# Optimization experiments

Hardware: AMD Instinct MI355X
Metric: run time of the kernel (lower is better)

The kernel has to match this reference:

```python
import jax, jax.numpy as jnp
import numpy as np

FEATURE_SIZE = 10 * 64 * 64  # 40960
HIDDEN1 = 512
HIDDEN2 = 256
BATCH = 4096


def setup_inputs() -> dict:
    key = jax.random.key(0)
    ks = jax.random.split(key, 8)
    # Sparse binary-ish features emulated as dense uniform (math is identical).
    white_features = jax.random.uniform(ks[0], (BATCH, FEATURE_SIZE), dtype=jnp.float32)
    black_features = jax.random.uniform(ks[1], (BATCH, FEATURE_SIZE), dtype=jnp.float32)
    s_ft = 1.0 / np.sqrt(FEATURE_SIZE)
    s_fc1 = 1.0 / np.sqrt(HIDDEN1 * 2)
    s_fc2 = 1.0 / np.sqrt(HIDDEN2)
    ft_w = jax.random.uniform(ks[2], (HIDDEN1, FEATURE_SIZE), minval=-s_ft, maxval=s_ft, dtype=jnp.float32)
    ft_b = jax.random.uniform(ks[3], (HIDDEN1,), minval=-s_ft, maxval=s_ft, dtype=jnp.float32)
    fc1_w = jax.random.uniform(ks[4], (HIDDEN2, HIDDEN1 * 2), minval=-s_fc1, maxval=s_fc1, dtype=jnp.float32)
    fc1_b = jax.random.uniform(ks[5], (HIDDEN2,), minval=-s_fc1, maxval=s_fc1, dtype=jnp.float32)
    fc2_w = jax.random.uniform(ks[6], (1, HIDDEN2), minval=-s_fc2, maxval=s_fc2, dtype=jnp.float32)
    fc2_b = jax.random.uniform(ks[7], (1,), minval=-s_fc2, maxval=s_fc2, dtype=jnp.float32)
    return dict(white_features=white_features, black_features=black_features,
                ft_w=ft_w, ft_b=ft_b, fc1_w=fc1_w, fc1_b=fc1_b, fc2_w=fc2_w, fc2_b=fc2_b)


def reference(white_features, black_features, ft_w, ft_b, fc1_w, fc1_b, fc2_w, fc2_b):
    # Feature transform per perspective, clamped to [0, 1]
    white_ft = jnp.clip(white_features @ ft_w.T + ft_b, 0.0, 1.0)  # [B, H1]
    black_ft = jnp.clip(black_features @ ft_w.T + ft_b, 0.0, 1.0)  # [B, H1]
    combined = jnp.concatenate([white_ft, black_ft], axis=1)       # [B, 2*H1]
    x = jax.nn.relu(combined @ fc1_w.T + fc1_b)                    # [B, H2]
    x = x @ fc2_w.T + fc2_b                                        # [B, 1]
    return x.squeeze(-1)
```

## Files before the change

kernel.cpp:

```cpp
#include <hip/hip_runtime.h>
#include <stdint.h>

#define BATCH 4096
#define FEAT  40960
#define H1    512
#define KS    4
#define KCHUNK (FEAT / KS)
#define NSTEPS (KCHUNK / 32)
#define NTILES (FEAT / 32)
#define WTILE  32768
#define WSLOT  32768
#define ALDS   65536

typedef float f32x4 __attribute__((ext_vector_type(4)));
typedef short s16x8 __attribute__((ext_vector_type(8)));
typedef unsigned int u32x2 __attribute__((ext_vector_type(2)));
typedef unsigned int u32x4 __attribute__((ext_vector_type(4)));

__device__ __forceinline__ unsigned bfpack2(float lo, float hi) {
  unsigned a = __float_as_uint(lo);
  unsigned b = __float_as_uint(hi);
  a += 0x7FFFu + ((a >> 16) & 1u);
  b += 0x7FFFu + ((b >> 16) & 1u);
  return (a >> 16) | (b & 0xFFFF0000u);
}

__device__ __forceinline__ int lds_swz(int r, int cb) {
  return (r << 6) + (cb ^ (((r >> 1) & 3) << 4));
}

__device__ __forceinline__ void glds16(const void* g, void* l) {
  __builtin_amdgcn_global_load_lds(
      (const __attribute__((address_space(1))) unsigned*)g,
      (__attribute__((address_space(3))) unsigned*)l, 16, 0, 0);
}

__global__ __launch_bounds__(512)
void wcvt_kernel(const float* __restrict__ ftw, char* __restrict__ wbf) {
  const int T = blockIdx.x;
  const int tid = threadIdx.x;
  const int c  = tid & 7;
  const int r0 = tid >> 3;
#pragma unroll
  for (int pass = 0; pass < 8; ++pass) {
    const int r = pass * 64 + r0;
    const float* src = ftw + (size_t)r * FEAT + T * 32 + c * 4;
    f32x4 v = *(const f32x4*)src;
    u32x2 o;
    o.x = bfpack2(v.x, v.y);
    o.y = bfpack2(v.z, v.w);
    const int nb = r >> 6, f = (r >> 4) & 3, lr = r & 15;
    const int l = (c >> 1) * 16 + lr;
    *(u32x2*)(wbf + (size_t)T * WTILE + ((nb * 4 + f) << 10) + l * 16 +
              (c & 1) * 8) = o;
  }
}

__global__ __launch_bounds__(512, 4)
void ft_gemm_kernel(const float* __restrict__ whiteF,
                    const float* __restrict__ blackF,
                    const char* __restrict__ wbf,
                    float* __restrict__ Ppart) {
  __shared__ char smem[73728];

  const int tid = threadIdx.x, bid = blockIdx.x;
  const int wgid = (bid & 7) * 64 + (bid >> 3);
  const int ks = wgid >> 7;
  const int p  = (wgid >> 6) & 1;
  const int mt = wgid & 63;

  const float* Ag =
      (p == 0 ? whiteF : blackF) + (size_t)(mt * 64) * FEAT + ks * KCHUNK;

  const int a_row = tid >> 3, a_kc = tid & 7;
  const float* aptr = Ag + (size_t)a_row * FEAT + a_kc * 4;
  const int awoff = lds_swz(a_row, a_kc * 8);

  const int lane = tid & 63, wave = tid >> 6;
  const int lrow = lane & 15, lkb = (lane >> 4) * 16;

  const char* wsrc =
      wbf + (size_t)ks * NSTEPS * WTILE + (wave << 12) + lane * 16;
  const int wofs = (wave << 12);

  int a_off[4];
#pragma unroll
  for (int m = 0; m < 4; ++m) a_off[m] = lds_swz(m * 16 + lrow, lkb);

  f32x4 acc[4][4];
#pragma unroll
  for (int m = 0; m < 4; ++m)
#pragma unroll
    for (int n = 0; n < 4; ++n) acc[m][n] = (f32x4){0.f, 0.f, 0.f, 0.f};

  f32x4 raA[2];

  raA[0] = *(const f32x4*)aptr;
  raA[1] = *(const f32x4*)(aptr + 32);
#pragma unroll
  for (int c = 0; c < 4; ++c)
    glds16(wsrc + c * 1024, smem + 0 * WSLOT + wofs + c * 1024);
#pragma unroll
  for (int c = 0; c < 4; ++c)
    glds16(wsrc + WTILE + c * 1024, smem + 1 * WSLOT + wofs + c * 1024);
  asm volatile("s_waitcnt vmcnt(9)" ::: "memory");
  __builtin_amdgcn_sched_barrier(0);
  {
    u32x2 av;
    av.x = bfpack2(raA[0].x, raA[0].y);
    av.y = bfpack2(raA[0].z, raA[0].w);
    *(u32x2*)(smem + ALDS + 0 * 4096 + awoff) = av;
  }
  raA[0] = *(const f32x4*)(aptr + 2 * 32);
  asm volatile("s_waitcnt lgkmcnt(0)" ::: "memory");
  __builtin_amdgcn_sched_barrier(0);
  __builtin_amdgcn_s_barrier();
  __builtin_amdgcn_sched_barrier(0);

#define GSTEP(B, t)                                                           \
  {                                                                           \
    asm volatile("s_waitcnt vmcnt(5)" ::: "memory");   \
    __builtin_amdgcn_sched_barrier(0);                                        \
    const char* wbase = smem + (B) * WSLOT + wofs;                            \
    const char* abase = smem + ALDS + (B) * 4096;                             \
    s16x8 af[4], wb[4];                                                       \
    _Pragma("unroll") for (int m = 0; m < 4; ++m)                             \
        af[m] = *(const s16x8*)(abase + a_off[m]);                            \
    _Pragma("unroll") for (int n = 0; n < 4; ++n)                             \
        wb[n] = *(const s16x8*)(wbase + n * 1024 + lane * 16);                \
    asm volatile("s_waitcnt lgkmcnt(0)" ::: "memory");      \
    __builtin_amdgcn_sched_barrier(0);                                        \
    {                     \
      const int t2 = ((t) + 2 < NSTEPS) ? (t) + 2 : NSTEPS - 1;               \
      const char* wsp = wsrc + (size_t)t2 * WTILE;                            \
      char* wdp = smem + (B) * WSLOT + wofs;                                  \
      _Pragma("unroll") for (int c = 0; c < 4; ++c)                           \
          glds16(wsp + c * 1024, wdp + c * 1024);                             \
    }                                                                         \
    {        \
      u32x2 av;                                                               \
      av.x = bfpack2(raA[(B) ^ 1].x, raA[(B) ^ 1].y);                         \
      av.y = bfpack2(raA[(B) ^ 1].z, raA[(B) ^ 1].w);                         \
      *(u32x2*)(smem + ALDS + ((B) ^ 1) * 4096 + awoff) = av;                 \
      const int t3 = ((t) + 3 < NSTEPS) ? (t) + 3 : NSTEPS - 1;               \
      raA[(B) ^ 1] = *(const f32x4*)(aptr + (size_t)t3 * 32);                 \
    }                                                                         \
    _Pragma("unroll") for (int n = 0; n < 4; ++n)                             \
      _Pragma("unroll") for (int m = 0; m < 4; ++m)                           \
          acc[m][n] = __builtin_amdgcn_mfma_f32_16x16x32_bf16(                \
              af[m], wb[n], acc[m][n], 0, 0, 0);                              \
    asm volatile("s_waitcnt lgkmcnt(0)" ::: "memory");   \
    __builtin_amdgcn_sched_barrier(0);                                        \
    __builtin_amdgcn_s_barrier();                                             \
    __builtin_amdgcn_sched_barrier(0);                                        \
  }

  for (int tt = 0; tt < NSTEPS; tt += 2) {
    GSTEP(0, tt);
    GSTEP(1, tt + 1);
  }
#undef GSTEP

  asm volatile("s_waitcnt vmcnt(0) lgkmcnt(0)" ::: "memory");
  __builtin_amdgcn_sched_barrier(0);

  float* Pp = Ppart + ((size_t)(ks * 2 + p) * BATCH + mt * 64) * H1;
  const int r0 = (lane >> 4) * 4;
  const int c0 = wave * 64 + lrow;
#pragma unroll
  for (int m = 0; m < 4; ++m)
#pragma unroll
    for (int n = 0; n < 4; ++n) {
      float* dst = Pp + (size_t)(r0 + m * 16) * H1 + c0 + n * 16;
#pragma unroll
      for (int j = 0; j < 4; ++j) dst[(size_t)j * H1] = acc[m][n][j];
    }
}

__global__ __launch_bounds__(256)
void ft_reduce_kernel(const float* __restrict__ Ppart,
                      const float* __restrict__ ftb,
                      unsigned short* __restrict__ comb) {
  const size_t gid = (size_t)blockIdx.x * 256 + threadIdx.x;
  const int    pp  = (int)(gid / (BATCH * H1 / 4));
  const size_t rem = gid % (BATCH * H1 / 4);
  const int    row = (int)(rem / (H1 / 4));
  const int    n4  = (int)(rem % (H1 / 4)) * 4;

  f32x4 s = (f32x4){0.f, 0.f, 0.f, 0.f};
#pragma unroll
  for (int ks = 0; ks < KS; ++ks)
    s += *(const f32x4*)(Ppart + ((size_t)(ks * 2 + pp) * BATCH + row) * H1 + n4);
  const f32x4 bv = *(const f32x4*)(ftb + n4);
  s += bv;
  s.x = fminf(fmaxf(s.x, 0.f), 1.f);
  s.y = fminf(fmaxf(s.y, 0.f), 1.f);
  s.z = fminf(fmaxf(s.z, 0.f), 1.f);
  s.w = fminf(fmaxf(s.w, 0.f), 1.f);

  u32x2 o;
  o.x = bfpack2(s.x, s.y);
  o.y = bfpack2(s.z, s.w);
  *(u32x2*)(comb + (size_t)row * 1024 + pp * H1 + n4) = o;
}

__global__ __launch_bounds__(256)
void fc_kernel(const unsigned short* __restrict__ comb,
               const float* __restrict__ w1, const float* __restrict__ b1,
               const float* __restrict__ w2, const float* __restrict__ b2,
               float* __restrict__ out) {
  __shared__ char smem[40960];
  __shared__ float rowsum[64];

  const int tid = threadIdx.x;
  const int bm  = blockIdx.x;
  if (tid < 64) rowsum[tid] = 0.f;

  const int a_row = tid >> 2, a_kq = tid & 3;
  const unsigned short* aptr = comb + (size_t)(bm * 64 + a_row) * 1024 + a_kq * 8;
  const float* wptr = w1 + (size_t)a_row * 1024 + a_kq * 8;

  u32x4 raA;
  f32x4 rw0[4], rw1[4];
  auto issue = [&](int t) {
    raA = *(const u32x4*)(aptr + t * 32);
    const float* wp = wptr + t * 32;
#pragma unroll
    for (int s = 0; s < 4; ++s) {
      rw0[s] = *(const f32x4*)(wp + (size_t)s * 64 * 1024);
      rw1[s] = *(const f32x4*)(wp + (size_t)s * 64 * 1024 + 4);
    }
  };

  const int aoff_w = lds_swz(a_row, a_kq * 16);
  int woff_w[4];
#pragma unroll
  for (int s = 0; s < 4; ++s)
    woff_w[s] = 4096 + lds_swz(s * 64 + a_row, a_kq * 16);

  auto cvtwrite = [&](int b) {
    char* base = smem + b * 20480;
    *(u32x4*)(base + aoff_w) = raA;
#pragma unroll
    for (int s = 0; s < 4; ++s) {
      u32x4 wv;
      wv.x = bfpack2(rw0[s].x, rw0[s].y); wv.y = bfpack2(rw0[s].z, rw0[s].w);
      wv.z = bfpack2(rw1[s].x, rw1[s].y); wv.w = bfpack2(rw1[s].z, rw1[s].w);
      *(u32x4*)(base + woff_w[s]) = wv;
    }
  };

  const int lane = tid & 63, wn = tid >> 6;
  const int lrow = lane & 15, lkb = (lane >> 4) * 16;
  int a_off[4], b_off[4];
#pragma unroll
  for (int m = 0; m < 4; ++m) a_off[m] = lds_swz(m * 16 + lrow, lkb);
#pragma unroll
  for (int n = 0; n < 4; ++n) b_off[n] = 4096 + lds_swz(wn * 64 + n * 16 + lrow, lkb);

  f32x4 acc[4][4];
#pragma unroll
  for (int m = 0; m < 4; ++m)
#pragma unroll
    for (int n = 0; n < 4; ++n) acc[m][n] = (f32x4){0.f, 0.f, 0.f, 0.f};

  issue(0);
  for (int t = 0; t < 32; ++t) {
    const int b = t & 1;
    cvtwrite(b);
    if (t + 1 < 32) issue(t + 1);
    asm volatile("s_waitcnt lgkmcnt(0)" ::: "memory");
    __builtin_amdgcn_sched_barrier(0);
    __builtin_amdgcn_s_barrier();
    __builtin_amdgcn_sched_barrier(0);
    char* base = smem + b * 20480;
    s16x8 af[4];
#pragma unroll
    for (int m = 0; m < 4; ++m) af[m] = *(const s16x8*)(base + a_off[m]);
#pragma unroll
    for (int n = 0; n < 4; ++n) {
      s16x8 bfn = *(const s16x8*)(base + b_off[n]);
#pragma unroll
      for (int m = 0; m < 4; ++m)
        acc[m][n] = __builtin_amdgcn_mfma_f32_16x16x32_bf16(af[m], bfn, acc[m][n], 0, 0, 0);
    }
  }

  float b1v[4], w2v[4];
#pragma unroll
  for (int n = 0; n < 4; ++n) {
    const int col = wn * 64 + n * 16 + lrow;
    b1v[n] = b1[col];
    w2v[n] = w2[col];
  }
#pragma unroll
  for (int m = 0; m < 4; ++m)
#pragma unroll
    for (int j = 0; j < 4; ++j) {
      float v = 0.f;
#pragma unroll
      for (int n = 0; n < 4; ++n) {
        float x = acc[m][n][j] + b1v[n];
        x = fmaxf(x, 0.f);
        v += x * w2v[n];
      }
#pragma unroll
      for (int d = 1; d < 16; d <<= 1) v += __shfl_xor(v, d, 64);
      if ((lane & 15) == 0)
        atomicAdd(&rowsum[m * 16 + (lane >> 4) * 4 + j], v);
    }
  __syncthreads();
  if (tid < 64) {
    out[bm * 64 + tid] = rowsum[tid] + b2[0];
  }
}

extern "C" void kernel_launch(void* const* d_in, const int* in_sizes, int n_in,
                              void* d_out, int out_size, void* d_ws, size_t ws_size,
                              hipStream_t stream) {
  const float* whiteF = (const float*)d_in[0];
  const float* blackF = (const float*)d_in[1];
  const float* ftw    = (const float*)d_in[2];
  const float* ftb    = (const float*)d_in[3];
  const float* w1     = (const float*)d_in[4];
  const float* b1     = (const float*)d_in[5];
  const float* w2     = (const float*)d_in[6];
  const float* b2     = (const float*)d_in[7];

  char* wbf = (char*)d_ws;
  const size_t wbf_bytes   = (size_t)NTILES * WTILE;
  const size_t ppart_bytes = (size_t)KS * 2 * BATCH * H1 * sizeof(float);
  float* Ppart = (float*)((char*)d_ws + wbf_bytes);
  unsigned short* comb = (unsigned short*)((char*)d_ws + wbf_bytes + ppart_bytes);
  float* outp = (float*)d_out;

  hipLaunchKernelGGL(wcvt_kernel, dim3(NTILES), dim3(512), 0, stream, ftw, wbf);
  hipLaunchKernelGGL(ft_gemm_kernel, dim3(512), dim3(512), 0, stream,
                     whiteF, blackF, wbf, Ppart);
  hipLaunchKernelGGL(ft_reduce_kernel, dim3((2 * BATCH * H1 / 4) / 256), dim3(256),
                     0, stream, Ppart, ftb, comb);
  hipLaunchKernelGGL(fc_kernel, dim3(BATCH / 64), dim3(256), 0, stream,
                     comb, w1, b1, w2, b2, outp);
}
```

Baseline: 541.6 us.

## Stage A in 128-wide K macro tiles to cut per-step workgroup barriers

The A (activation) tile now covers 128 K columns and lives in a single swizzled LDS buffer. It is loaded from global memory once per macro step and converted to bf16 mid-macro. Because each wave streams its own private W slots, the four inner 32-K micro steps no longer need a workgroup barrier, leaving two barriers per macro step instead of one per 32-K step. The trade-offs are more LDS, more registers for the prefetched A rows, and less overlap of the A store with compute.

Result: slower. 1.183 ms (+118.5%).

```diff
diff --git a/kernel.cpp b/kernel.cpp
--- a/kernel.cpp
+++ b/kernel.cpp
@@ -7,10 +7,11 @@
 #define KS    4
 #define KCHUNK (FEAT / KS)
 #define NSTEPS (KCHUNK / 32)
+#define NMACRO (KCHUNK / 128)
 #define NTILES (FEAT / 32)
 #define WTILE  32768
 #define WSLOT  32768
-#define ALDS   65536
+#define AOFF   65536
 
 typedef float f32x4 __attribute__((ext_vector_type(4)));
 typedef short s16x8 __attribute__((ext_vector_type(8)));
@@ -61,7 +62,7 @@
                     const float* __restrict__ blackF,
                     const char* __restrict__ wbf,
                     float* __restrict__ Ppart) {
-  __shared__ char smem[73728];
+  __shared__ char smem[81920];
 
   const int tid = threadIdx.x, bid = blockIdx.x;
   const int wgid = (bid & 7) * 64 + (bid >> 3);
@@ -72,100 +73,119 @@
   const float* Ag =
       (p == 0 ? whiteF : blackF) + (size_t)(mt * 64) * FEAT + ks * KCHUNK;
 
-  const int a_row = tid >> 3, a_kc = tid & 7;
-  const float* aptr = Ag + (size_t)a_row * FEAT + a_kc * 4;
-  const int awoff = lds_swz(a_row, a_kc * 8);
-
   const int lane = tid & 63, wave = tid >> 6;
-  const int lrow = lane & 15, lkb = (lane >> 4) * 16;
+  const int lrow = lane & 15, lkq = lane >> 4;
+
+  const int arow = wave * 8 + (lane >> 5);
+  const int l31 = lane & 31;
+  const float* abase = Ag + (size_t)arow * FEAT + l31 * 4;
+  int awr[4];
+#pragma unroll
+  for (int j = 0; j < 4; ++j) {
+    const int r = arow + 2 * j;
+    awr[j] = AOFF + r * 256 + (((l31 >> 1) ^ (r & 7)) << 4) + (l31 & 1) * 8;
+  }
+  const int rx7 = lrow & 7;
+  int ard[4];
+#pragma unroll
+  for (int i = 0; i < 4; ++i) ard[i] = AOFF + (i * 16 + lrow) * 256;
 
   const char* wsrc =
       wbf + (size_t)ks * NSTEPS * WTILE + (wave << 12) + lane * 16;
   const int wofs = (wave << 12);
 
-  int a_off[4];
-#pragma unroll
-  for (int m = 0; m < 4; ++m) a_off[m] = lds_swz(m * 16 + lrow, lkb);
-
   f32x4 acc[4][4];
 #pragma unroll
   for (int m = 0; m < 4; ++m)
 #pragma unroll
     for (int n = 0; n < 4; ++n) acc[m][n] = (f32x4){0.f, 0.f, 0.f, 0.f};
 
-  f32x4 raA[2];
-
-  raA[0] = *(const f32x4*)aptr;
-  raA[1] = *(const f32x4*)(aptr + 32);
+  f32x4 raf[4];
+  u32x2 ab[4];
+
+#pragma unroll
+  for (int j = 0; j < 4; ++j) raf[j] = *(const f32x4*)(abase + 2 * j * FEAT);
 #pragma unroll
   for (int c = 0; c < 4; ++c)
     glds16(wsrc + c * 1024, smem + 0 * WSLOT + wofs + c * 1024);
 #pragma unroll
   for (int c = 0; c < 4; ++c)
     glds16(wsrc + WTILE + c * 1024, smem + 1 * WSLOT + wofs + c * 1024);
-  asm volatile("s_waitcnt vmcnt(9)" ::: "memory");
+  asm volatile("s_waitcnt vmcnt(8)" ::: "memory");
   __builtin_amdgcn_sched_barrier(0);
-  {
-    u32x2 av;
-    av.x = bfpack2(raA[0].x, raA[0].y);
-    av.y = bfpack2(raA[0].z, raA[0].w);
-    *(u32x2*)(smem + ALDS + 0 * 4096 + awoff) = av;
-  }
-  raA[0] = *(const f32x4*)(aptr + 2 * 32);
+#pragma unroll
+  for (int j = 0; j < 4; ++j) {
+    ab[j].x = bfpack2(raf[j].x, raf[j].y);
+    ab[j].y = bfpack2(raf[j].z, raf[j].w);
+    *(u32x2*)(smem + awr[j]) = ab[j];
+  }
   asm volatile("s_waitcnt lgkmcnt(0)" ::: "memory");
   __builtin_amdgcn_sched_barrier(0);
   __builtin_amdgcn_s_barrier();
   __builtin_amdgcn_sched_barrier(0);
 
-#define GSTEP(B, t)                                                           \
+#define MICRO(M, SLOT, WAITN, DO_RAF, DO_CVT, T)                              \
   {                                                                           \
-    asm volatile("s_waitcnt vmcnt(5)" ::: "memory");   \
+    asm volatile("s_waitcnt vmcnt(" #WAITN ")" ::: "memory");                 \
     __builtin_amdgcn_sched_barrier(0);                                        \
-    const char* wbase = smem + (B) * WSLOT + wofs;                            \
-    const char* abase = smem + ALDS + (B) * 4096;                             \
+    if (DO_RAF) {                                                             \
+      const int Tn = ((T) + 1 < NMACRO) ? (T) + 1 : NMACRO - 1;               \
+      const float* ap = abase + (size_t)Tn * 128;                             \
+      _Pragma("unroll") for (int j = 0; j < 4; ++j)                           \
+          raf[j] = *(const f32x4*)(ap + 2 * j * FEAT);                        \
+    }                                                                         \
+    if (DO_CVT) {                                                             \
+      _Pragma("unroll") for (int j = 0; j < 4; ++j) {                         \
+        ab[j].x = bfpack2(raf[j].x, raf[j].y);                                \
+        ab[j].y = bfpack2(raf[j].z, raf[j].w);                                \
+      }                                                                       \
+    }                                                                         \
+    const char* wbase = smem + (SLOT) * WSLOT + wofs;                         \
     s16x8 af[4], wb[4];                                                       \
-    _Pragma("unroll") for (int m = 0; m < 4; ++m)                             \
-        af[m] = *(const s16x8*)(abase + a_off[m]);                            \
+    _Pragma("unroll") for (int i = 0; i < 4; ++i)                             \
+        af[i] = *(const s16x8*)(smem + ard[i] +                               \
+                                ((((M) * 4 + lkq) ^ rx7) << 4));              \
     _Pragma("unroll") for (int n = 0; n < 4; ++n)                             \
         wb[n] = *(const s16x8*)(wbase + n * 1024 + lane * 16);                \
-    asm volatile("s_waitcnt lgkmcnt(0)" ::: "memory");      \
+    asm volatile("s_waitcnt lgkmcnt(0)" ::: "memory");                        \
     __builtin_amdgcn_sched_barrier(0);                                        \
-    {                     \
-      const int t2 = ((t) + 2 < NSTEPS) ? (t) + 2 : NSTEPS - 1;               \
-      const char* wsp = wsrc + (size_t)t2 * WTILE;                            \
-      char* wdp = smem + (B) * WSLOT + wofs;                                  \
+    {                                 \
+      const int u2 = (4 * (T) + (M) + 2 < NSTEPS) ? 4 * (T) + (M) + 2         \
+                                                  : NSTEPS - 1;               \
+      const char* wsp = wsrc + (size_t)u2 * WTILE;                            \
+      char* wdp = smem + (SLOT) * WSLOT + wofs;                               \
       _Pragma("unroll") for (int c = 0; c < 4; ++c)                           \
           glds16(wsp + c * 1024, wdp + c * 1024);                             \
     }                                                                         \
-    {        \
-      u32x2 av;                                                               \
-      av.x = bfpack2(raA[(B) ^ 1].x, raA[(B) ^ 1].y);                         \
-      av.y = bfpack2(raA[(B) ^ 1].z, raA[(B) ^ 1].w);                         \
-      *(u32x2*)(smem + ALDS + ((B) ^ 1) * 4096 + awoff) = av;                 \
-      const int t3 = ((t) + 3 < NSTEPS) ? (t) + 3 : NSTEPS - 1;               \
-      raA[(B) ^ 1] = *(const f32x4*)(aptr + (size_t)t3 * 32);                 \
-    }                                                                         \
     _Pragma("unroll") for (int n = 0; n < 4; ++n)                             \
-      _Pragma("unroll") for (int m = 0; m < 4; ++m)                           \
-          acc[m][n] = __builtin_amdgcn_mfma_f32_16x16x32_bf16(                \
-              af[m], wb[n], acc[m][n], 0, 0, 0);                              \
-    asm volatile("s_waitcnt lgkmcnt(0)" ::: "memory");   \
-    __builtin_amdgcn_sched_barrier(0);                                        \
-    __builtin_amdgcn_s_barrier();                                             \
-    __builtin_amdgcn_sched_barrier(0);                                        \
-  }
-
-  for (int tt = 0; tt < NSTEPS; tt += 2) {
-    GSTEP(0, tt);
-    GSTEP(1, tt + 1);
-  }
-#undef GSTEP
+      _Pragma("unroll") for (int i = 0; i < 4; ++i)                           \
+          acc[i][n] = __builtin_amdgcn_mfma_f32_16x16x32_bf16(                \
+              af[i], wb[n], acc[i][n], 0, 0, 0);                              \
+  }
+
+  for (int T = 0; T < NMACRO; ++T) {
+    MICRO(0, 0, 4, true, false, T);
+    MICRO(1, 1, 8, false, false, T);
+    MICRO(2, 0, 4, false, true, T);
+    MICRO(3, 1, 4, false, false, T);
+    asm volatile("s_waitcnt lgkmcnt(0)" ::: "memory");
+    __builtin_amdgcn_sched_barrier(0);
+    __builtin_amdgcn_s_barrier();
+    __builtin_amdgcn_sched_barrier(0);
+#pragma unroll
+    for (int j = 0; j < 4; ++j) *(u32x2*)(smem + awr[j]) = ab[j];
+    asm volatile("s_waitcnt lgkmcnt(0)" ::: "memory");
+    __builtin_amdgcn_sched_barrier(0);
+    __builtin_amdgcn_s_barrier();
+    __builtin_amdgcn_sched_barrier(0);
+  }
+#undef MICRO
 
   asm volatile("s_waitcnt vmcnt(0) lgkmcnt(0)" ::: "memory");
   __builtin_amdgcn_sched_barrier(0);
 
   float* Pp = Ppart + ((size_t)(ks * 2 + p) * BATCH + mt * 64) * H1;
-  const int r0 = (lane >> 4) * 4;
+  const int r0 = lkq * 4;
   const int c0 = wave * 64 + lrow;
 #pragma unroll
   for (int m = 0; m < 4; ++m)
```

## Split FT GEMM tiles along N into 64x128 blocks with smaller LDS

Applied to the files above, without the earlier changes.

The feature-transform GEMM moves from 512-thread blocks computing 64x512 output tiles to 256-thread blocks computing 64x128 tiles, with 2048 blocks and an XCD-aware mapping that keeps each perspective and K split on one XCD. LDS use drops from 72KB to 24KB so more blocks fit per CU, and the weight layout in the conversion kernel is flattened to 16-row column blocks. The intent is better occupancy and latency hiding. The cost is that every A tile (fp32 activations, the dominant traffic) is now loaded and converted four times, once per N tile, instead of once, which may raise global and L2 traffic.

Result: slower. 772.6 us (+42.7%).

```diff
diff --git a/kernel.cpp b/kernel.cpp
--- a/kernel.cpp
+++ b/kernel.cpp
@@ -9,8 +9,8 @@
 #define NSTEPS (KCHUNK / 32)
 #define NTILES (FEAT / 32)
 #define WTILE  32768
-#define WSLOT  32768
-#define ALDS   65536
+#define WSLOT  8192
+#define ABASE  16384
 
 typedef float f32x4 __attribute__((ext_vector_type(4)));
 typedef short s16x8 __attribute__((ext_vector_type(8)));
@@ -49,69 +49,68 @@
     u32x2 o;
     o.x = bfpack2(v.x, v.y);
     o.y = bfpack2(v.z, v.w);
-    const int nb = r >> 6, f = (r >> 4) & 3, lr = r & 15;
+    const int cb = r >> 4, lr = r & 15;
     const int l = (c >> 1) * 16 + lr;
-    *(u32x2*)(wbf + (size_t)T * WTILE + ((nb * 4 + f) << 10) + l * 16 +
-              (c & 1) * 8) = o;
-  }
-}
-
-__global__ __launch_bounds__(512, 4)
+    *(u32x2*)(wbf + (size_t)T * WTILE + (cb << 10) + l * 16 + (c & 1) * 8) = o;
+  }
+}
+
+__global__ __launch_bounds__(256, 6)
 void ft_gemm_kernel(const float* __restrict__ whiteF,
                     const float* __restrict__ blackF,
                     const char* __restrict__ wbf,
                     float* __restrict__ Ppart) {
-  __shared__ char smem[73728];
+  __shared__ char smem[24576];
 
   const int tid = threadIdx.x, bid = blockIdx.x;
-  const int wgid = (bid & 7) * 64 + (bid >> 3);
-  const int ks = wgid >> 7;
-  const int p  = (wgid >> 6) & 1;
-  const int mt = wgid & 63;
+  const int xcd = bid & 7, idx = bid >> 3;
+  const int p  = xcd & 1;
+  const int ks = xcd >> 1;
+  const int nt = idx & 3;
+  const int mt = idx >> 2;
 
   const float* Ag =
       (p == 0 ? whiteF : blackF) + (size_t)(mt * 64) * FEAT + ks * KCHUNK;
 
-  const int a_row = tid >> 3, a_kc = tid & 7;
-  const float* aptr = Ag + (size_t)a_row * FEAT + a_kc * 4;
-  const int awoff = lds_swz(a_row, a_kc * 8);
-
-  const int lane = tid & 63, wave = tid >> 6;
-  const int lrow = lane & 15, lkb = (lane >> 4) * 16;
-
-  const char* wsrc =
-      wbf + (size_t)ks * NSTEPS * WTILE + (wave << 12) + lane * 16;
-  const int wofs = (wave << 12);
+  const int a_row = tid >> 2, a_kc = tid & 3;
+  const float* aptr = Ag + (size_t)a_row * FEAT + a_kc * 8;
+  const int awoff = lds_swz(a_row, a_kc * 16);
+
+  const int lane = tid & 63, wn = tid >> 6;
+  const int lrow = lane & 15, lkq = lane >> 4;
+
+  const int cb = (nt * 4 + wn) * 2;
+  const char* wsrc = wbf + (size_t)ks * NSTEPS * WTILE + (cb << 10) + lane * 16;
+  const int wofs = wn * 2048;
 
   int a_off[4];
 #pragma unroll
-  for (int m = 0; m < 4; ++m) a_off[m] = lds_swz(m * 16 + lrow, lkb);
-
-  f32x4 acc[4][4];
+  for (int m = 0; m < 4; ++m) a_off[m] = lds_swz(m * 16 + lrow, lkq * 16);
+
+  f32x4 acc[4][2];
 #pragma unroll
   for (int m = 0; m < 4; ++m)
 #pragma unroll
-    for (int n = 0; n < 4; ++n) acc[m][n] = (f32x4){0.f, 0.f, 0.f, 0.f};
-
-  f32x4 raA[2];
-
-  raA[0] = *(const f32x4*)aptr;
-  raA[1] = *(const f32x4*)(aptr + 32);
-#pragma unroll
-  for (int c = 0; c < 4; ++c)
+    for (int n = 0; n < 2; ++n) acc[m][n] = (f32x4){0.f, 0.f, 0.f, 0.f};
+
+  f32x4 raA0, raA1;
+
+  raA0 = *(const f32x4*)aptr;
+  raA1 = *(const f32x4*)(aptr + 4);
+#pragma unroll
+  for (int c = 0; c < 2; ++c)
     glds16(wsrc + c * 1024, smem + 0 * WSLOT + wofs + c * 1024);
 #pragma unroll
-  for (int c = 0; c < 4; ++c)
+  for (int c = 0; c < 2; ++c)
     glds16(wsrc + WTILE + c * 1024, smem + 1 * WSLOT + wofs + c * 1024);
-  asm volatile("s_waitcnt vmcnt(9)" ::: "memory");
-  __builtin_amdgcn_sched_barrier(0);
   {
-    u32x2 av;
-    av.x = bfpack2(raA[0].x, raA[0].y);
-    av.y = bfpack2(raA[0].z, raA[0].w);
-    *(u32x2*)(smem + ALDS + 0 * 4096 + awoff) = av;
-  }
-  raA[0] = *(const f32x4*)(aptr + 2 * 32);
+    u32x4 av;
+    av.x = bfpack2(raA0.x, raA0.y); av.y = bfpack2(raA0.z, raA0.w);
+    av.z = bfpack2(raA1.x, raA1.y); av.w = bfpack2(raA1.z, raA1.w);
+    *(u32x4*)(smem + ABASE + 0 * 4096 + awoff) = av;
+  }
+  raA0 = *(const f32x4*)(aptr + 32);
+  raA1 = *(const f32x4*)(aptr + 36);
   asm volatile("s_waitcnt lgkmcnt(0)" ::: "memory");
   __builtin_amdgcn_sched_barrier(0);
   __builtin_amdgcn_s_barrier();
@@ -119,33 +118,33 @@
 
 #define GSTEP(B, t)                                                           \
   {                                                                           \
-    asm volatile("s_waitcnt vmcnt(5)" ::: "memory");   \
+    asm volatile("s_waitcnt vmcnt(4)" ::: "memory");         \
     __builtin_amdgcn_sched_barrier(0);                                        \
     const char* wbase = smem + (B) * WSLOT + wofs;                            \
-    const char* abase = smem + ALDS + (B) * 4096;                             \
-    s16x8 af[4], wb[4];                                                       \
+    const char* abase = smem + ABASE + (B) * 4096;                            \
+    s16x8 af[4], wb[2];                                                       \
     _Pragma("unroll") for (int m = 0; m < 4; ++m)                             \
         af[m] = *(const s16x8*)(abase + a_off[m]);                            \
-    _Pragma("unroll") for (int n = 0; n < 4; ++n)                             \
+    _Pragma("unroll") for (int n = 0; n < 2; ++n)                             \
         wb[n] = *(const s16x8*)(wbase + n * 1024 + lane * 16);                \
     asm volatile("s_waitcnt lgkmcnt(0)" ::: "memory");      \
     __builtin_amdgcn_sched_barrier(0);                                        \
-    {                     \
+    {                   \
+      u32x4 av;                                                               \
+      av.x = bfpack2(raA0.x, raA0.y); av.y = bfpack2(raA0.z, raA0.w);         \
+      av.z = bfpack2(raA1.x, raA1.y); av.w = bfpack2(raA1.z, raA1.w);         \
+      *(u32x4*)(smem + ABASE + ((B) ^ 1) * 4096 + awoff) = av;                \
+    }                                                                         \
+    {        \
       const int t2 = ((t) + 2 < NSTEPS) ? (t) + 2 : NSTEPS - 1;               \
+      raA0 = *(const f32x4*)(aptr + (size_t)t2 * 32);                         \
+      raA1 = *(const f32x4*)(aptr + (size_t)t2 * 32 + 4);                     \
       const char* wsp = wsrc + (size_t)t2 * WTILE;                            \
       char* wdp = smem + (B) * WSLOT + wofs;                                  \
-      _Pragma("unroll") for (int c = 0; c < 4; ++c)                           \
+      _Pragma("unroll") for (int c = 0; c < 2; ++c)                           \
           glds16(wsp + c * 1024, wdp + c * 1024);                             \
     }                                                                         \
-    {        \
-      u32x2 av;                                                               \
-      av.x = bfpack2(raA[(B) ^ 1].x, raA[(B) ^ 1].y);                         \
-      av.y = bfpack2(raA[(B) ^ 1].z, raA[(B) ^ 1].w);                         \
-      *(u32x2*)(smem + ALDS + ((B) ^ 1) * 4096 + awoff) = av;                 \
-      const int t3 = ((t) + 3 < NSTEPS) ? (t) + 3 : NSTEPS - 1;               \
-      raA[(B) ^ 1] = *(const f32x4*)(aptr + (size_t)t3 * 32);                 \
-    }                                                                         \
-    _Pragma("unroll") for (int n = 0; n < 4; ++n)                             \
+    _Pragma("unroll") for (int n = 0; n < 2; ++n)                             \
       _Pragma("unroll") for (int m = 0; m < 4; ++m)                           \
           acc[m][n] = __builtin_amdgcn_mfma_f32_16x16x32_bf16(                \
               af[m], wb[n], acc[m][n], 0, 0, 0);                              \
@@ -165,12 +164,12 @@
   __builtin_amdgcn_sched_barrier(0);
 
   float* Pp = Ppart + ((size_t)(ks * 2 + p) * BATCH + mt * 64) * H1;
-  const int r0 = (lane >> 4) * 4;
-  const int c0 = wave * 64 + lrow;
+  const int r0 = lkq * 4;
+  const int c0 = nt * 128 + wn * 32 + lrow;
 #pragma unroll
   for (int m = 0; m < 4; ++m)
 #pragma unroll
-    for (int n = 0; n < 4; ++n) {
+    for (int n = 0; n < 2; ++n) {
       float* dst = Pp + (size_t)(r0 + m * 16) * H1 + c0 + n * 16;
 #pragma unroll
       for (int j = 0; j < 4; ++j) dst[(size_t)j * H1] = acc[m][n][j];
@@ -335,7 +334,7 @@
   float* outp = (float*)d_out;
 
   hipLaunchKernelGGL(wcvt_kernel, dim3(NTILES), dim3(512), 0, stream, ftw, wbf);
-  hipLaunchKernelGGL(ft_gemm_kernel, dim3(512), dim3(512), 0, stream,
+  hipLaunchKernelGGL(ft_gemm_kernel, dim3(2048), dim3(256), 0, stream,
                      whiteF, blackF, wbf, Ppart);
   hipLaunchKernelGGL(ft_reduce_kernel, dim3((2 * BATCH * H1 / 4) / 256), dim3(256),
                      0, stream, Ppart, ftb, comb);
```
